# Kernel tuning notes

Measured on AMD Instinct MI355X. Metric: run time of the kernel, lower is better.

The kernel has to match this reference:

```python
import jax, jax.numpy as jnp
import numpy as np

T, B, H, E, V = 128, 64, 512, 256, 32000
UNK = 2
EPS = 1e-10


def setup_inputs() -> dict:
    key = jax.random.key(0)
    ks = jax.random.split(key, 16)
    s = 0.02
    return {
        "u_enc_out": jax.random.normal(ks[0], (T, B, H), jnp.float32),
        "z_tm1": jax.random.randint(ks[1], (1, B), 0, V),
        "last_hidden": jax.random.normal(ks[2], (1, B, H), jnp.float32),
        "u_input": jax.random.randint(ks[3], (T, B), 0, V),
        "emb": jax.random.normal(ks[4], (V, E), jnp.float32) * s,
        "attn_W": jax.random.normal(ks[5], (H, 2 * H), jnp.float32) * s,
        "attn_b": jnp.zeros((H,), jnp.float32),
        "attn_v": jax.random.normal(ks[6], (H,), jnp.float32) * (1.0 / np.sqrt(H)),
        "gru_Wih": jax.random.normal(ks[7], (3 * H, H + E), jnp.float32) * s,
        "gru_Whh": jax.random.normal(ks[8], (3 * H, H), jnp.float32) * s,
        "gru_bih": jnp.zeros((3 * H,), jnp.float32),
        "gru_bhh": jnp.zeros((3 * H,), jnp.float32),
        "proj_W": jax.random.normal(ks[9], (V, 2 * H), jnp.float32) * s,
        "proj_b": jnp.zeros((V,), jnp.float32),
        "copy1_W": jax.random.normal(ks[10], (H, H), jnp.float32) * s,
        "copy1_b": jnp.zeros((H,), jnp.float32),
    }


def _copy_logscore(raw, u_input):
    # raw: [B,T] copy scores; u_input: [T,B] int ids
    # Faithful to: log(bmm(exp(raw - max), sparse_one_hot_with_1e-10_floor)) + max
    cmax = jnp.max(raw, axis=1, keepdims=True)            # [B,1]
    ex = jnp.exp(raw - cmax)                              # [B,T]
    idx = u_input.T                                       # [B,T]
    idx = jnp.where(idx == UNK, V + jnp.arange(T)[None, :], idx)
    mask = (u_input.T != 0).astype(ex.dtype)
    total = jnp.sum(ex, axis=1)                           # [B] (all t, incl. ignored)
    scat = jax.vmap(lambda e, i: jnp.zeros((V + T,), ex.dtype).at[i].add(e))(ex * mask, idx)
    return jnp.log(EPS * total[:, None] + (1.0 - EPS) * scat) + cmax  # [B,V+T]


def reference(u_enc_out, z_tm1, last_hidden, u_input, emb, attn_W, attn_b, attn_v,
              gru_Wih, gru_Whh, gru_bih, gru_bhh, proj_W, proj_b, copy1_W, copy1_b):
    enc = jnp.transpose(u_enc_out, (1, 0, 2))             # [B,T,H]
    h = last_hidden[0]                                    # [B,H]
    # Attn: energy = tanh(Linear([h;enc])), score = v . energy, softmax over T
    Hrep = jnp.broadcast_to(h[:, None, :], enc.shape)
    energy = jnp.tanh(jnp.einsum('bti,hi->bth', jnp.concatenate([Hrep, enc], -1), attn_W) + attn_b)
    alpha = jax.nn.softmax(jnp.einsum('h,bth->bt', attn_v, energy), axis=1)
    ctx = jnp.einsum('bt,bth->bh', alpha, enc)            # [B,H]
    # GRU step (pytorch gate order r,z,n)
    x = jnp.concatenate([emb[z_tm1[0]], ctx], axis=-1)    # [B,E+H]
    gi = x @ gru_Wih.T + gru_bih
    gh = h @ gru_Whh.T + gru_bhh
    i_r, i_z, i_n = jnp.split(gi, 3, axis=-1)
    h_r, h_z, h_n = jnp.split(gh, 3, axis=-1)
    r = jax.nn.sigmoid(i_r + h_r)
    z = jax.nn.sigmoid(i_z + h_z)
    n = jnp.tanh(i_n + r * h_n)
    h_new = (1.0 - z) * n + z * h                         # [B,H]
    gru_out = h_new[None]                                 # [1,B,H]
    new_hidden = h_new[None]
    # generation score
    gen_score = jnp.concatenate([h_new, ctx], -1) @ proj_W.T + proj_b  # [B,V]
    # copy score
    cs = jnp.tanh(jnp.einsum('bth,ih->bti', enc, copy1_W) + copy1_b)   # [B,T,H]
    raw = jnp.einsum('bth,bh->bt', cs, h_new)             # [B,T]
    u_copy = _copy_logscore(raw, u_input)                 # [B,V+T]
    scores = jax.nn.softmax(jnp.concatenate([gen_score, u_copy], axis=1), axis=1)
    g, c = scores[:, :V], scores[:, V:]                   # [B,V], [B,V+T]
    proba = jnp.concatenate([g + c[:, :V], c[:, V:]], axis=1)  # [B,V+T]
    return gru_out, new_hidden, proba
```

## Files before the change

kernel.cpp:

```cpp
#include <hip/hip_runtime.h>
#include <math.h>

#define T_ 128
#define B_ 64
#define H_ 512
#define E_ 256
#define V_ 32000
#define VT_ (V_ + T_)
#define UNK_ 2
#define EPS_ 1e-10f
#define NP_ (V_ / 64)

typedef __attribute__((ext_vector_type(8))) _Float16 half8;
typedef __attribute__((ext_vector_type(4))) float floatx4;

#define NB_ZERO 32
#define NB_CVTE 2048
#define NB_CVTA 512
#define NB_CVTC 512
#define NB_WH   8192
#define NB_CVTW 2048
#define NB_XE   64
#define NB_XH   128
#define NB_BC   8
#define NB_PRO (NB_ZERO + NB_CVTE + NB_CVTA + NB_CVTC + NB_WH + NB_CVTW + NB_XE + NB_XH + NB_BC)

__global__ __launch_bounds__(256) void prologue_k(
        const float* __restrict__ u_enc, const float* __restrict__ attn_W,
        const float* __restrict__ copy1_W, const float* __restrict__ last_h,
        const float* __restrict__ attn_b, const float* __restrict__ emb,
        const int* __restrict__ z, const float* __restrict__ Wih,
        const float* __restrict__ Whh, const float* __restrict__ bih,
        const float* __restrict__ bhh,
        float* __restrict__ zbase, _Float16* __restrict__ enc_h,
        _Float16* __restrict__ Wb_attn, _Float16* __restrict__ Wb_copy,
        float* __restrict__ Wh, _Float16* __restrict__ Wcat,
        _Float16* __restrict__ xg, float* __restrict__ bcat) {
    int bid = blockIdx.x, tid = threadIdx.x;
    if (bid < NB_ZERO) { zbase[bid * 256 + tid] = 0.f; return; }
    bid -= NB_ZERO;
    if (bid < NB_CVTE) {
        int i = (bid * 256 + tid) * 8;
        float4 a = *(const float4*)(u_enc + i);
        float4 b = *(const float4*)(u_enc + i + 4);
        half8 o;
        o[0] = (_Float16)a.x; o[1] = (_Float16)a.y; o[2] = (_Float16)a.z; o[3] = (_Float16)a.w;
        o[4] = (_Float16)b.x; o[5] = (_Float16)b.y; o[6] = (_Float16)b.z; o[7] = (_Float16)b.w;
        *(half8*)(enc_h + i) = o;
        return;
    }
    bid -= NB_CVTE;
    if (bid < NB_CVTA) {
        int c = tid * 2;
        float2 v = *(const float2*)(attn_W + (size_t)bid * 1024 + 512 + c);
        Wb_attn[bid * 512 + c]     = (_Float16)v.x;
        Wb_attn[bid * 512 + c + 1] = (_Float16)v.y;
        return;
    }
    bid -= NB_CVTA;
    if (bid < NB_CVTC) {
        int c = tid * 2;
        float2 v = *(const float2*)(copy1_W + (size_t)bid * 512 + c);
        Wb_copy[bid * 512 + c]     = (_Float16)v.x;
        Wb_copy[bid * 512 + c + 1] = (_Float16)v.y;
        return;
    }
    bid -= NB_CVTC;
    if (bid < NB_WH) {
        int wid = bid * 4 + (tid >> 6), lane = tid & 63;
        int b = wid >> 9, m = wid & 511;
        const float4* wr = (const float4*)(attn_W + (size_t)m * 1024);
        const float4* xr = (const float4*)(last_h + b * 512);
        float s = 0.f;
        #pragma unroll
        for (int i = 0; i < 2; ++i) {
            int k = lane + i * 64;
            float4 w = wr[k], x = xr[k];
            s += w.x * x.x + w.y * x.y + w.z * x.z + w.w * x.w;
        }
        #pragma unroll
        for (int off = 32; off > 0; off >>= 1) s += __shfl_down(s, off);
        if (lane == 0) Wh[b * 512 + m] = s + attn_b[m];
        return;
    }
    bid -= NB_WH;
    if (bid < NB_CVTW) {
        int mp = bid;
        int q  = (mp >> 4) & 3;
        int hh = (mp >> 6) * 16 + (mp & 15);
        #pragma unroll
        for (int j = 0; j < 5; ++j) {
            int c = j * 256 + tid;
            float w;
            if (q == 0)      w = (c < 768) ? Wih[(size_t)hh * 768 + c]
                                           : Whh[(size_t)hh * 512 + (c - 768)];
            else if (q == 1) w = (c < 768) ? Wih[(size_t)(512 + hh) * 768 + c]
                                           : Whh[(size_t)(512 + hh) * 512 + (c - 768)];
            else if (q == 2) w = (c < 768) ? Wih[(size_t)(1024 + hh) * 768 + c] : 0.f;
            else             w = (c >= 768) ? Whh[(size_t)(1024 + hh) * 512 + (c - 768)] : 0.f;
            Wcat[(size_t)mp * 1280 + c] = (_Float16)w;
        }
        return;
    }
    bid -= NB_CVTW;
    if (bid < NB_XE) {
        int idx = bid * 256 + tid;
        int bb = idx >> 8, c = idx & 255;
        xg[bb * 1280 + c] = (_Float16)emb[(size_t)z[bb] * E_ + c];
        return;
    }
    bid -= NB_XE;
    if (bid < NB_XH) {
        int idx = bid * 256 + tid;
        int bb = idx >> 9, c = idx & 511;
        xg[bb * 1280 + 768 + c] = (_Float16)last_h[bb * H_ + c];
        return;
    }
    bid -= NB_XH;
    {
        int mp = bid * 256 + tid;
        int q  = (mp >> 4) & 3;
        int hh = (mp >> 6) * 16 + (mp & 15);
        float v2;
        if (q == 0)      v2 = bih[hh] + bhh[hh];
        else if (q == 1) v2 = bih[512 + hh] + bhh[512 + hh];
        else if (q == 2) v2 = bih[1024 + hh];
        else             v2 = bhh[1024 + hh];
        bcat[mp] = v2;
    }
}

__global__ __launch_bounds__(256) void enc_dual_k(
        const _Float16* __restrict__ enc_h,
        const _Float16* __restrict__ Wa,
        const _Float16* __restrict__ Wc,
        const float* __restrict__ Wh,
        const float* __restrict__ attn_v,
        const float* __restrict__ copy1_b,
        float* __restrict__ score,
        _Float16* __restrict__ cs) {
    int lane = threadIdx.x & 63;
    int wave = threadIdx.x >> 6;
    int r0 = blockIdx.x * 64;
    int b  = r0 / T_;
    int t0 = r0 % T_;
    int n0 = blockIdx.y * 64 + wave * 16;
    int coln = lane & 15;
    int kq   = (lane >> 4) * 8;
    const _Float16* wra = Wa + (size_t)(n0 + coln) * H_ + kq;
    const _Float16* wrc = Wc + (size_t)(n0 + coln) * H_ + kq;
    floatx4 acca[4] = {}, accc[4] = {};
    #pragma unroll 4
    for (int k0 = 0; k0 < H_; k0 += 32) {
        half8 fba = *(const half8*)(wra + k0);
        half8 fbc = *(const half8*)(wrc + k0);
        #pragma unroll
        for (int mi = 0; mi < 4; ++mi) {
            const _Float16* arow = enc_h +
                ((size_t)(t0 + mi * 16 + coln) * B_ + b) * H_ + k0 + kq;
            half8 fa = *(const half8*)arow;
            acca[mi] = __builtin_amdgcn_mfma_f32_16x16x32_f16(fa, fba, acca[mi], 0, 0, 0);
            accc[mi] = __builtin_amdgcn_mfma_f32_16x16x32_f16(fa, fbc, accc[mi], 0, 0, 0);
        }
    }
    int col = n0 + coln;
    float addt = Wh[b * H_ + col];
    float av   = attn_v[col];
    float cb   = copy1_b[col];
    int rbase = (lane >> 4) * 4;
    #pragma unroll
    for (int mi = 0; mi < 4; ++mi)
        #pragma unroll
        for (int r = 0; r < 4; ++r) {
            int row = r0 + mi * 16 + rbase + r;
            float x = acca[mi][r] + addt;
            float t2 = __expf(2.f * x);
            float v = av * ((t2 - 1.f) / (t2 + 1.f));
            v += __shfl_xor(v, 1);
            v += __shfl_xor(v, 2);
            v += __shfl_xor(v, 4);
            v += __shfl_xor(v, 8);
            if (coln == 0) atomicAdd(&score[row], v);
            float y = accc[mi][r] + cb;
            float t3 = __expf(2.f * y);
            cs[(size_t)row * H_ + col] = (_Float16)((t3 - 1.f) / (t3 + 1.f));
        }
}

__global__ __launch_bounds__(256) void softctx_k(
        const float* __restrict__ score, const _Float16* __restrict__ enc_h,
        _Float16* __restrict__ xcat, _Float16* __restrict__ xg) {
    __shared__ float al[T_];
    __shared__ float red[T_];
    int b = blockIdx.x, tid = threadIdx.x;
    float v = (tid < T_) ? score[b * T_ + tid] : -1e30f;
    if (tid < T_) red[tid] = v;
    __syncthreads();
    for (int s = 64; s > 0; s >>= 1) { if (tid < s) red[tid] = fmaxf(red[tid], red[tid + s]); __syncthreads(); }
    float m = red[0]; __syncthreads();
    float e = (tid < T_) ? __expf(v - m) : 0.f;
    if (tid < T_) red[tid] = e;
    __syncthreads();
    for (int s = 64; s > 0; s >>= 1) { if (tid < s) red[tid] += red[tid + s]; __syncthreads(); }
    if (tid < T_) al[tid] = e / red[0];
    __syncthreads();
    int h = blockIdx.y * 256 + tid;
    float s2 = 0.f;
    #pragma unroll 4
    for (int t = 0; t < T_; ++t) s2 += al[t] * (float)enc_h[((size_t)t * B_ + b) * H_ + h];
    xcat[b * 1024 + 512 + h] = (_Float16)s2;
    xg[b * 1280 + 256 + h]   = (_Float16)s2;
}

__global__ __launch_bounds__(256) void grucat_k(
        const _Float16* __restrict__ xg,
        const _Float16* __restrict__ Wcat,
        const float* __restrict__ bcat,
        const float* __restrict__ hprev,
        float* __restrict__ out,
        _Float16* __restrict__ xcat) {
    __shared__ float Lt[4][64][16];
    int lane = threadIdx.x & 63;
    int wave = threadIdx.x >> 6;
    int n0 = blockIdx.x * 64 + wave * 16;
    int coln = lane & 15;
    int kq  = (lane >> 4) * 8;
    const _Float16* wrow = Wcat + (size_t)(n0 + coln) * 1280 + kq;
    const _Float16* abase = xg + kq;
    floatx4 acc[4] = {};
    #pragma unroll 8
    for (int k0 = 0; k0 < 1280; k0 += 32) {
        half8 fb = *(const half8*)(wrow + k0);
        #pragma unroll
        for (int mi = 0; mi < 4; ++mi) {
            half8 fa = *(const half8*)(abase + (size_t)(mi * 16 + coln) * 1280 + k0);
            acc[mi] = __builtin_amdgcn_mfma_f32_16x16x32_f16(fa, fb, acc[mi], 0, 0, 0);
        }
    }
    int rbase = (lane >> 4) * 4;
    float bias = bcat[n0 + coln];
    #pragma unroll
    for (int mi = 0; mi < 4; ++mi)
        #pragma unroll
        for (int r = 0; r < 4; ++r)
            Lt[wave][mi * 16 + rbase + r][coln] = acc[mi][r] + bias;
    __syncthreads();
    int HB = blockIdx.x * 16;
    #pragma unroll
    for (int p = threadIdx.x; p < 1024; p += 256) {
        int b = p >> 4, i = p & 15;
        float rr = 1.f / (1.f + __expf(-Lt[0][b][i]));
        float zz = 1.f / (1.f + __expf(-Lt[1][b][i]));
        float nn = tanhf(Lt[2][b][i] + rr * Lt[3][b][i]);
        float h  = hprev[b * H_ + HB + i];
        float hv = (1.f - zz) * nn + zz * h;
        out[b * H_ + HB + i] = hv;
        out[B_ * H_ + b * H_ + HB + i] = hv;
        xcat[b * 1024 + HB + i] = (_Float16)hv;
    }
}

__global__ __launch_bounds__(256) void proj_stats_k(
        const _Float16* __restrict__ xcat,
        const float* __restrict__ Wp,
        const float* __restrict__ bp,
        float* __restrict__ gen,
        float* __restrict__ mpart, float* __restrict__ lpart) {
    __shared__ float m_lds[4][64];
    __shared__ float l_lds[4][64];
    int lane = threadIdx.x & 63;
    int wave = threadIdx.x >> 6;
    int n0 = (blockIdx.x * 4 + wave) * 16;
    int coln = lane & 15;
    int kq  = (lane >> 4) * 8;
    const float* wrow = Wp + (size_t)(n0 + coln) * 1024 + kq;
    const _Float16* abase = xcat + kq;
    floatx4 acc[4] = {};
    #pragma unroll 8
    for (int k0 = 0; k0 < 1024; k0 += 32) {
        const float4* wb = (const float4*)(wrow + k0);
        float4 w0 = wb[0], w1 = wb[1];
        half8 fb;
        fb[0] = (_Float16)w0.x; fb[1] = (_Float16)w0.y; fb[2] = (_Float16)w0.z; fb[3] = (_Float16)w0.w;
        fb[4] = (_Float16)w1.x; fb[5] = (_Float16)w1.y; fb[6] = (_Float16)w1.z; fb[7] = (_Float16)w1.w;
        #pragma unroll
        for (int mi = 0; mi < 4; ++mi) {
            half8 fa = *(const half8*)(abase + (size_t)(mi * 16 + coln) * 1024 + k0);
            acc[mi] = __builtin_amdgcn_mfma_f32_16x16x32_f16(fa, fb, acc[mi], 0, 0, 0);
        }
    }
    int rbase = (lane >> 4) * 4;
    float bias = bp[n0 + coln];
    #pragma unroll
    for (int mi = 0; mi < 4; ++mi)
        #pragma unroll
        for (int r = 0; r < 4; ++r) {
            int brow = mi * 16 + rbase + r;
            float x = acc[mi][r] + bias;
            gen[(size_t)brow * V_ + n0 + coln] = x;
            float mm = x;
            mm = fmaxf(mm, __shfl_xor(mm, 1));
            mm = fmaxf(mm, __shfl_xor(mm, 2));
            mm = fmaxf(mm, __shfl_xor(mm, 4));
            mm = fmaxf(mm, __shfl_xor(mm, 8));
            float e = __expf(x - mm);
            e += __shfl_xor(e, 1);
            e += __shfl_xor(e, 2);
            e += __shfl_xor(e, 4);
            e += __shfl_xor(e, 8);
            if (coln == 0) { m_lds[wave][brow] = mm; l_lds[wave][brow] = e; }
        }
    __syncthreads();
    if (threadIdx.x < 64) {
        int bb = threadIdx.x;
        float M = m_lds[0][bb], L = l_lds[0][bb];
        #pragma unroll
        for (int w = 1; w < 4; ++w) {
            float m2 = m_lds[w][bb], l2 = l_lds[w][bb];
            float nm = fmaxf(M, m2);
            L = L * __expf(M - nm) + l2 * __expf(m2 - nm);
            M = nm;
        }
        mpart[bb * NP_ + blockIdx.x] = M;
        lpart[bb * NP_ + blockIdx.x] = L;
    }
}

__global__ __launch_bounds__(256) void raw_epi_k(
        const _Float16* __restrict__ cs, const float* __restrict__ hnew,
        const int* __restrict__ u_input,
        const float* __restrict__ mpart, const float* __restrict__ lpart,
        float* __restrict__ scat, float* __restrict__ params) {
    __shared__ float rawS[T_];
    __shared__ float red[T_];
    __shared__ float ms[256], ls[256];
    int b = blockIdx.x, tid = threadIdx.x;
    int lane = tid & 63, wave = tid >> 6;
    const float4* hp = (const float4*)(hnew + b * H_ + lane * 8);
    float4 ha = hp[0], hb = hp[1];
    #pragma unroll 4
    for (int i = 0; i < 32; ++i) {
        int t = wave * 32 + i;
        half8 c8 = *(const half8*)(cs + (size_t)(b * T_ + t) * H_ + lane * 8);
        float s = (float)c8[0] * ha.x + (float)c8[1] * ha.y + (float)c8[2] * ha.z + (float)c8[3] * ha.w
                + (float)c8[4] * hb.x + (float)c8[5] * hb.y + (float)c8[6] * hb.z + (float)c8[7] * hb.w;
        #pragma unroll
        for (int off = 32; off > 0; off >>= 1) s += __shfl_down(s, off);
        if (lane == 0) rawS[t] = s;
    }
    __syncthreads();
    int t = tid;
    float v = (t < T_) ? rawS[t] : -1e30f;
    if (t < T_) red[t] = v;
    __syncthreads();
    for (int s = 64; s > 0; s >>= 1) { if (t < s) red[t] = fmaxf(red[t], red[t + s]); __syncthreads(); }
    float cm = red[0]; __syncthreads();
    float e = (t < T_) ? __expf(v - cm) : 0.f;
    if (t < T_) red[t] = e;
    __syncthreads();
    for (int s = 64; s > 0; s >>= 1) { if (t < s) red[t] += red[t + s]; __syncthreads(); }
    float tot = red[0]; __syncthreads();
    int id = (t < T_) ? u_input[t * B_ + b] : 0;
    size_t j = (size_t)b * VT_ + ((id == UNK_) ? (V_ + t) : id);
    if (id != 0) scat[j] = 0.f;
    __syncthreads();
    if (id != 0) atomicAdd(&scat[j], e);
    if (t < T_) red[t] = (id != 0) ? e : 0.f;
    __syncthreads();
    for (int s = 64; s > 0; s >>= 1) { if (t < s) red[t] += red[t + s]; __syncthreads(); }
    float ssum = red[0]; __syncthreads();
    float sv = (id != 0) ? scat[j] : 0.f;
    if (t < T_) red[t] = sv;
    __syncthreads();
    for (int s = 64; s > 0; s >>= 1) { if (t < s) red[t] = fmaxf(red[t], red[t + s]); __syncthreads(); }
    float smax = red[0]; __syncthreads();
    float M = -1e30f, L = 0.f;
    for (int s = t; s < NP_; s += 256) {
        float m2 = mpart[b * NP_ + s], l2 = lpart[b * NP_ + s];
        float nm = fmaxf(M, m2);
        L = L * __expf(M - nm) + l2 * __expf(m2 - nm);
        M = nm;
    }
    ms[t] = M; ls[t] = L;
    __syncthreads();
    for (int s = 128; s > 0; s >>= 1) {
        if (t < s) {
            float m2 = ms[t + s], l2 = ls[t + s];
            float nm = fmaxf(ms[t], m2);
            ls[t] = ls[t] * __expf(ms[t] - nm) + l2 * __expf(m2 - nm);
            ms[t] = nm;
        }
        __syncthreads();
    }
    if (t == 0) {
        float Mg = ms[0], Zg = ls[0];
        float umax = cm + logf(EPS_ * tot + (1.f - EPS_) * smax);
        float M2 = fmaxf(Mg, umax);
        float coef = __expf(cm - M2);
        float Z = Zg * __expf(Mg - M2) + coef * (EPS_ * tot * (float)VT_ + (1.f - EPS_) * ssum);
        float invZ = 1.f / Z;
        params[b * 4 + 0] = M2;
        params[b * 4 + 1] = invZ;
        params[b * 4 + 2] = coef * EPS_ * tot * invZ;
        params[b * 4 + 3] = coef * (1.f - EPS_) * invZ;
    }
}

__global__ __launch_bounds__(256) void write_k(const float* __restrict__ gen,
                                               const float* __restrict__ params,
                                               float* __restrict__ proba) {
    int b = blockIdx.y;
    int i4 = blockIdx.x * 256 + threadIdx.x;
    if (i4 >= VT_ / 4) return;
    float M = params[b * 4], invZ = params[b * 4 + 1], addc = params[b * 4 + 2];
    int j = i4 * 4;
    float4 p;
    if (j < V_) {
        float4 g = *(const float4*)(gen + (size_t)b * V_ + j);
        p.x = addc + __expf(g.x - M) * invZ;
        p.y = addc + __expf(g.y - M) * invZ;
        p.z = addc + __expf(g.z - M) * invZ;
        p.w = addc + __expf(g.w - M) * invZ;
    } else {
        p.x = p.y = p.z = p.w = addc;
    }
    *(float4*)(proba + (size_t)b * VT_ + j) = p;
}

__global__ void fix_k(const float* __restrict__ gen, const float* __restrict__ scat,
                      const int* __restrict__ u_input, const float* __restrict__ params,
                      float* __restrict__ proba) {
    int b = blockIdx.x, t = threadIdx.x;
    int id = u_input[t * B_ + b];
    if (id == 0) return;
    int j = (id == UNK_) ? (V_ + t) : id;
    float M = params[b * 4], invZ = params[b * 4 + 1];
    float addc = params[b * 4 + 2], scoef = params[b * 4 + 3];
    float p = addc + scoef * scat[(size_t)b * VT_ + j];
    if (j < V_) p += __expf(gen[(size_t)b * V_ + j] - M) * invZ;
    proba[(size_t)b * VT_ + j] = p;
}

extern "C" void kernel_launch(void* const* d_in, const int* in_sizes, int n_in,
                              void* d_out, int out_size, void* d_ws, size_t ws_size,
                              hipStream_t stream) {
    const float* u_enc   = (const float*)d_in[0];
    const int*   z_tm1   = (const int*)d_in[1];
    const float* last_h  = (const float*)d_in[2];
    const int*   u_input = (const int*)d_in[3];
    const float* emb     = (const float*)d_in[4];
    const float* attn_W  = (const float*)d_in[5];
    const float* attn_b  = (const float*)d_in[6];
    const float* attn_v  = (const float*)d_in[7];
    const float* gru_Wih = (const float*)d_in[8];
    const float* gru_Whh = (const float*)d_in[9];
    const float* gru_bih = (const float*)d_in[10];
    const float* gru_bhh = (const float*)d_in[11];
    const float* proj_W  = (const float*)d_in[12];
    const float* proj_b  = (const float*)d_in[13];
    const float* copy1_W = (const float*)d_in[14];
    const float* copy1_b = (const float*)d_in[15];
    float* out = (float*)d_out;

    float* ws    = (float*)d_ws;
    float* score = ws;
    float* gen   = score + B_ * T_;
    float* scat  = gen + (size_t)B_ * V_;
    float* Wh    = scat + (size_t)B_ * VT_;
    float* mpart = Wh + B_ * H_;
    float* lpart = mpart + B_ * NP_;
    float* params= lpart + B_ * NP_;
    float* bcat  = params + B_ * 4;
    _Float16* xcat  = (_Float16*)(bcat + 2048);
    _Float16* xg    = xcat + B_ * 1024;
    _Float16* enc_h = xg + B_ * 1280;
    _Float16* Wb_attn = enc_h + (size_t)T_ * B_ * H_;
    _Float16* Wb_copy = Wb_attn + H_ * H_;
    _Float16* Wcat  = Wb_copy + H_ * H_;
    _Float16* cs    = Wcat + 2048 * 1280;

    prologue_k<<<NB_PRO, 256, 0, stream>>>(u_enc, attn_W, copy1_W, last_h, attn_b,
                                           emb, z_tm1, gru_Wih, gru_Whh, gru_bih, gru_bhh,
                                           score, enc_h, Wb_attn, Wb_copy, Wh, Wcat, xg, bcat);

    dim3 g2(T_ * B_ / 64, H_ / 64);
    enc_dual_k<<<g2, 256, 0, stream>>>(enc_h, Wb_attn, Wb_copy, Wh, attn_v, copy1_b,
                                       score, cs);

    softctx_k<<<dim3(B_, 2), 256, 0, stream>>>(score, enc_h, xcat, xg);

    grucat_k<<<2048 / 64, 256, 0, stream>>>(xg, Wcat, bcat, last_h, out, xcat);

    proj_stats_k<<<NP_, 256, 0, stream>>>(xcat, proj_W, proj_b, gen, mpart, lpart);

    raw_epi_k<<<B_, 256, 0, stream>>>(cs, out, u_input, mpart, lpart, scat, params);

    float* proba = out + 2 * B_ * H_;
    write_k<<<dim3((VT_ / 4 + 255) / 256, B_), 256, 0, stream>>>(gen, params, proba);
    fix_k<<<B_, T_, 0, stream>>>(gen, scat, u_input, params, proba);
}
```

Before: 393.2 us.

## Transpose encoder to batch-major, stage A tile in swizzled LDS, remap blocks per XCD

The prologue now writes the fp16 encoder in [B,T,H] order instead of [T,B,H]. This makes each 64-row tile of enc_dual_k one contiguous 64 KB region, which the kernel copies into XOR-swizzled shared memory before the MFMA loop. Before, every A fragment was a strided global load, and the four column-tile blocks each reloaded the same rows. A 1D grid remaps block IDs so blocks sharing the same rows land on the same XCD for L2 reuse. The 64 KB LDS tile per block limits occupancy, and softctx now reads encoder rows contiguously per batch.

```diff
diff --git a/kernel.cpp b/kernel.cpp
--- a/kernel.cpp
+++ b/kernel.cpp
@@ -32,7 +32,7 @@
         const int* __restrict__ z, const float* __restrict__ Wih,
         const float* __restrict__ Whh, const float* __restrict__ bih,
         const float* __restrict__ bhh,
-        float* __restrict__ zbase, _Float16* __restrict__ enc_h,
+        float* __restrict__ zbase, _Float16* __restrict__ enc_bh,
         _Float16* __restrict__ Wb_attn, _Float16* __restrict__ Wb_copy,
         float* __restrict__ Wh, _Float16* __restrict__ Wcat,
         _Float16* __restrict__ xg, float* __restrict__ bcat) {
@@ -40,13 +40,17 @@
     if (bid < NB_ZERO) { zbase[bid * 256 + tid] = 0.f; return; }
     bid -= NB_ZERO;
     if (bid < NB_CVTE) {
-        int i = (bid * 256 + tid) * 8;
+        int idx8 = bid * 256 + tid;
+        int i = idx8 * 8;
         float4 a = *(const float4*)(u_enc + i);
-        float4 b = *(const float4*)(u_enc + i + 4);
+        float4 b4 = *(const float4*)(u_enc + i + 4);
         half8 o;
         o[0] = (_Float16)a.x; o[1] = (_Float16)a.y; o[2] = (_Float16)a.z; o[3] = (_Float16)a.w;
-        o[4] = (_Float16)b.x; o[5] = (_Float16)b.y; o[6] = (_Float16)b.z; o[7] = (_Float16)b.w;
-        *(half8*)(enc_h + i) = o;
+        o[4] = (_Float16)b4.x; o[5] = (_Float16)b4.y; o[6] = (_Float16)b4.z; o[7] = (_Float16)b4.w;
+        int h8 = idx8 & 63;
+        int tb = idx8 >> 6;
+        int b = tb & 63, t = tb >> 6;
+        *(half8*)(enc_bh + ((size_t)(b * T_ + t) * H_) + h8 * 8) = o;
         return;
     }
     bid -= NB_CVTE;
@@ -131,7 +135,7 @@
 }
 
 __global__ __launch_bounds__(256) void enc_dual_k(
-        const _Float16* __restrict__ enc_h,
+        const _Float16* __restrict__ enc_bh,
         const _Float16* __restrict__ Wa,
         const _Float16* __restrict__ Wc,
         const float* __restrict__ Wh,
@@ -139,16 +143,29 @@
         const float* __restrict__ copy1_b,
         float* __restrict__ score,
         _Float16* __restrict__ cs) {
-    int lane = threadIdx.x & 63;
-    int wave = threadIdx.x >> 6;
-    int r0 = blockIdx.x * 64;
-    int b  = r0 / T_;
-    int t0 = r0 % T_;
-    int n0 = blockIdx.y * 64 + wave * 16;
+    __shared__ _Float16 As[64 * 512];
+    int bid = blockIdx.x;
+    int xcd = bid & 7, loc = bid >> 3;
+    int xt = xcd * 16 + (loc & 15);
+    int yt = loc >> 4;
+    int r0 = xt * 64;
+    int b  = r0 >> 7;
+    int tid = threadIdx.x;
+    int lane = tid & 63, wave = tid >> 6;
+    const half8* src = (const half8*)(enc_bh + (size_t)r0 * H_);
+    #pragma unroll
+    for (int i = 0; i < 16; ++i) {
+        int G = i * 256 + tid;
+        half8 v = src[G];
+        int r = G >> 6, s = G & 63;
+        *(half8*)&As[(size_t)(((r << 6) | (s ^ (r & 7))) << 3)] = v;
+    }
+    __syncthreads();
+    int n0 = yt * 64 + wave * 16;
     int coln = lane & 15;
-    int kq   = (lane >> 4) * 8;
-    const _Float16* wra = Wa + (size_t)(n0 + coln) * H_ + kq;
-    const _Float16* wrc = Wc + (size_t)(n0 + coln) * H_ + kq;
+    int g = lane >> 4;
+    const _Float16* wra = Wa + (size_t)(n0 + coln) * H_ + g * 8;
+    const _Float16* wrc = Wc + (size_t)(n0 + coln) * H_ + g * 8;
     floatx4 acca[4] = {}, accc[4] = {};
     #pragma unroll 4
     for (int k0 = 0; k0 < H_; k0 += 32) {
@@ -156,9 +173,9 @@
         half8 fbc = *(const half8*)(wrc + k0);
         #pragma unroll
         for (int mi = 0; mi < 4; ++mi) {
-            const _Float16* arow = enc_h +
-                ((size_t)(t0 + mi * 16 + coln) * B_ + b) * H_ + k0 + kq;
-            half8 fa = *(const half8*)arow;
+            int r = mi * 16 + coln;
+            half8 fa = *(const half8*)&As[((size_t)r << 9) +
+                          ((((k0 >> 3) + g) ^ (coln & 7)) << 3)];
             acca[mi] = __builtin_amdgcn_mfma_f32_16x16x32_f16(fa, fba, acca[mi], 0, 0, 0);
             accc[mi] = __builtin_amdgcn_mfma_f32_16x16x32_f16(fa, fbc, accc[mi], 0, 0, 0);
         }
@@ -167,7 +184,7 @@
     float addt = Wh[b * H_ + col];
     float av   = attn_v[col];
     float cb   = copy1_b[col];
-    int rbase = (lane >> 4) * 4;
+    int rbase = g * 4;
     #pragma unroll
     for (int mi = 0; mi < 4; ++mi)
         #pragma unroll
@@ -188,7 +205,7 @@
 }
 
 __global__ __launch_bounds__(256) void softctx_k(
-        const float* __restrict__ score, const _Float16* __restrict__ enc_h,
+        const float* __restrict__ score, const _Float16* __restrict__ enc_bh,
         _Float16* __restrict__ xcat, _Float16* __restrict__ xg) {
     __shared__ float al[T_];
     __shared__ float red[T_];
@@ -207,7 +224,7 @@
     int h = blockIdx.y * 256 + tid;
     float s2 = 0.f;
     #pragma unroll 4
-    for (int t = 0; t < T_; ++t) s2 += al[t] * (float)enc_h[((size_t)t * B_ + b) * H_ + h];
+    for (int t = 0; t < T_; ++t) s2 += al[t] * (float)enc_bh[((size_t)b * T_ + t) * H_ + h];
     xcat[b * 1024 + 512 + h] = (_Float16)s2;
     xg[b * 1280 + 256 + h]   = (_Float16)s2;
 }
@@ -473,21 +490,20 @@
     float* bcat  = params + B_ * 4;
     _Float16* xcat  = (_Float16*)(bcat + 2048);
     _Float16* xg    = xcat + B_ * 1024;
-    _Float16* enc_h = xg + B_ * 1280;
-    _Float16* Wb_attn = enc_h + (size_t)T_ * B_ * H_;
+    _Float16* enc_bh = xg + B_ * 1280;
+    _Float16* Wb_attn = enc_bh + (size_t)T_ * B_ * H_;
     _Float16* Wb_copy = Wb_attn + H_ * H_;
     _Float16* Wcat  = Wb_copy + H_ * H_;
     _Float16* cs    = Wcat + 2048 * 1280;
 
     prologue_k<<<NB_PRO, 256, 0, stream>>>(u_enc, attn_W, copy1_W, last_h, attn_b,
                                            emb, z_tm1, gru_Wih, gru_Whh, gru_bih, gru_bhh,
-                                           score, enc_h, Wb_attn, Wb_copy, Wh, Wcat, xg, bcat);
-
-    dim3 g2(T_ * B_ / 64, H_ / 64);
-    enc_dual_k<<<g2, 256, 0, stream>>>(enc_h, Wb_attn, Wb_copy, Wh, attn_v, copy1_b,
-                                       score, cs);
-
-    softctx_k<<<dim3(B_, 2), 256, 0, stream>>>(score, enc_h, xcat, xg);
+                                           score, enc_bh, Wb_attn, Wb_copy, Wh, Wcat, xg, bcat);
+
+    enc_dual_k<<<1024, 256, 0, stream>>>(enc_bh, Wb_attn, Wb_copy, Wh, attn_v, copy1_b,
+                                         score, cs);
+
+    softctx_k<<<dim3(B_, 2), 256, 0, stream>>>(score, enc_bh, xcat, xg);
 
     grucat_k<<<2048 / 64, 256, 0, stream>>>(xg, Wcat, bcat, last_h, out, xcat);
 
```

Measured after the change: 372.7 us. 1.06x faster.
